# Kernel optimization log

Measured on AMD Instinct MI355X. Metric: run time of the kernel, lower is better.

## Reference

```python
import jax, jax.numpy as jnp
import numpy as np

T = 64        # n_estimators
DEPTH = 8
D = 2**DEPTH - 1   # internal nodes per tree (255)
K = 2**DEPTH       # leaves per tree (256)
M = 512       # n_features
C = 8         # class_num
B = 4096      # batch


def _build_path_masks():
    # Complete binary tree in heap order. For leaf l, walk from root;
    # going LEFT corresponds to b==+1 -> multiply (1 - x_node) -> Bpos,
    # going RIGHT corresponds to b==-1 -> multiply x_node -> Bneg.
    Bpos = np.zeros((K, D), dtype=np.float32)
    Bneg = np.zeros((K, D), dtype=np.float32)
    for l in range(K):
        node = 0
        for level in range(DEPTH):
            bit = (l >> (DEPTH - 1 - level)) & 1
            if bit == 0:
                Bpos[l, node] = 1.0
            else:
                Bneg[l, node] = 1.0
            node = 2 * node + 1 + bit
    return Bpos, Bneg


def setup_inputs() -> dict:
    rng = np.random.default_rng(0)
    key = jax.random.key(0)
    x = jax.random.normal(key, (B, M), dtype=jnp.float32)
    # fcn1: each internal node splits on one feature -> one-hot weight row,
    # bias = -threshold (change_parameters1).
    feat = rng.integers(0, M, size=(T, D))
    W1 = np.zeros((T, D, M), dtype=np.float32)
    W1[np.arange(T)[:, None], np.arange(D)[None, :], feat] = 1.0
    b1 = (-rng.standard_normal((T, D))).astype(np.float32)  # -threshold
    # Path masks shared across trees (complete trees), tiled per tree.
    Bpos1, Bneg1 = _build_path_masks()
    Bpos = np.broadcast_to(Bpos1, (T, K, D)).copy()
    Bneg = np.broadcast_to(Bneg1, (T, K, D)).copy()
    # fcn2 weight = c^T with zero bias (change_parameters2): leaf values [T, K, C]
    Cw = rng.random((T, K, C)).astype(np.float32)
    return {
        "input": x,
        "W1": jnp.asarray(W1),
        "b1": jnp.asarray(b1),
        "Bpos": jnp.asarray(Bpos),
        "Bneg": jnp.asarray(Bneg),
        "Cw": jnp.asarray(Cw),
    }


def reference(input, W1, b1, Bpos, Bneg, Cw):
    # z: [B, T, D] = 10 * (fcn1 per tree)
    z = 10.0 * (jnp.einsum("bm,tdm->btd", input, W1) + b1)
    # x = sigmoid(z); leaf-path product:
    #   x_c[b,t,k] = prod_d x^Bneg[t,k,d] * (1-x)^Bpos[t,k,d]
    # computed exactly in log-space (all factors in (0,1)):
    log_x = jax.nn.log_sigmoid(z)       # log sigmoid(z)
    log_1mx = jax.nn.log_sigmoid(-z)    # log (1 - sigmoid(z))
    log_xc = (jnp.einsum("btd,tkd->btk", log_x, Bneg)
              + jnp.einsum("btd,tkd->btk", log_1mx, Bpos))
    x_c = jnp.exp(log_xc)               # [B, T, K]
    # fcn2 (zero bias) then forest average over trees
    out = jnp.einsum("btk,tkc->bc", x_c, Cw) / T
    return out
```

## Files before the change

### kernel.cpp

```cpp
#include <hip/hip_runtime.h>
#include <hip/hip_bf16.h>

#define TT 64
#define DD 255
#define KK 256
#define MM 512
#define CC 8
#define BB 4096
#define NB 4
#define TPB 32
#define TG 4

typedef _Float16 h2 __attribute__((ext_vector_type(2)));

__device__ __forceinline__ float wave_sum(float v) {
    v += __shfl_down(v, 32, 64);
    v += __shfl_down(v, 16, 64);
    v += __shfl_down(v, 8, 64);
    v += __shfl_down(v, 4, 64);
    v += __shfl_down(v, 2, 64);
    v += __shfl_down(v, 1, 64);
    return v;
}

__global__ void feat_kernel(const float* __restrict__ W1, int* __restrict__ feat) {
    const int row = blockIdx.x * 4 + (threadIdx.x >> 6);
    const int lane = threadIdx.x & 63;
    const float4* r = reinterpret_cast<const float4*>(W1 + (size_t)row * MM);
    float4 a = r[lane];
    float4 b = r[lane + 64];
    float ba = (float)(4 * lane);
    float bb = (float)(4 * (lane + 64));
    float acc = 0.0f;
    acc = fmaf(a.x, ba,        acc);
    acc = fmaf(a.y, ba + 1.0f, acc);
    acc = fmaf(a.z, ba + 2.0f, acc);
    acc = fmaf(a.w, ba + 3.0f, acc);
    acc = fmaf(b.x, bb,        acc);
    acc = fmaf(b.y, bb + 1.0f, acc);
    acc = fmaf(b.z, bb + 2.0f, acc);
    acc = fmaf(b.w, bb + 3.0f, acc);
    acc = wave_sum(acc);
    if (lane == 0) feat[row] = (int)(acc + 0.5f);
}

__device__ __forceinline__ float sigm_from(float xv, float c1) {
    float earg = fmaf(-14.426950408889634f, xv, c1);
    float e = exp2f(earg);
    return __builtin_amdgcn_rcpf(1.0f + e);
}

__global__ __launch_bounds__(256, 2) void forest_kernel(
        const float* __restrict__ x, const float* __restrict__ b1,
        const float* __restrict__ Cw, const int* __restrict__ feat,
        float* __restrict__ out) {
    __shared__ float xsi[MM][NB];
    __shared__ h2 s8[NB * 2 * 256];
    __shared__ float red[4][NB][CC];

    const int tid = threadIdx.x;
    const int b0 = blockIdx.x * NB;
    const int t0 = blockIdx.y * TPB;

    for (int idx = tid; idx < MM * NB; idx += 256) {
        int m = idx & (MM - 1);
        int bl = idx >> 9;
        xsi[m][bl] = x[(size_t)(b0 + bl) * MM + m];
    }

    h2 acc[NB][4];
    #pragma unroll
    for (int bl = 0; bl < NB; ++bl)
        #pragma unroll
        for (int q = 0; q < 4; ++q)
            acc[bl][q] = (h2){(_Float16)0.0f, (_Float16)0.0f};

    const int i = tid & 127;
    const int sub = tid >> 7;
    const h2 one = {(_Float16)1.0f, (_Float16)1.0f};

    for (int g = 0; g < TPB / TG; ++g) {
        __syncthreads();
        if (tid < DD) {
            const int d = tid;
            int f[TG];
            float c1[TG];
            #pragma unroll
            for (int j = 0; j < TG; ++j) {
                int t = t0 + g * TG + j;
                f[j] = feat[t * DD + d];
                c1[j] = -14.426950408889634f * b1[t * DD + d];
            }
            float sv[NB][TG];
            #pragma unroll
            for (int j = 0; j < TG; ++j) {
                float4 xv = *reinterpret_cast<const float4*>(&xsi[f[j]][0]);
                sv[0][j] = sigm_from(xv.x, c1[j]);
                sv[1][j] = sigm_from(xv.y, c1[j]);
                sv[2][j] = sigm_from(xv.z, c1[j]);
                sv[3][j] = sigm_from(xv.w, c1[j]);
            }
            #pragma unroll
            for (int bl = 0; bl < NB; ++bl) {
                s8[(bl * 2 + 0) * 256 + d] =
                    (h2){(_Float16)sv[bl][0], (_Float16)sv[bl][1]};
                s8[(bl * 2 + 1) * 256 + d] =
                    (h2){(_Float16)sv[bl][2], (_Float16)sv[bl][3]};
            }
        }
        __syncthreads();

        h2 cwa[2][4], cwb[2][4];
        #pragma unroll
        for (int j = 0; j < 2; ++j) {
            int t = t0 + g * TG + sub * 2 + j;
            const float4* p = reinterpret_cast<const float4*>(
                Cw + ((size_t)t * KK + 2 * i) * CC);
            float4 a0 = p[0], a1 = p[1], bv0 = p[2], bv1 = p[3];
            cwa[j][0] = (h2){(_Float16)a0.x, (_Float16)a0.y};
            cwa[j][1] = (h2){(_Float16)a0.z, (_Float16)a0.w};
            cwa[j][2] = (h2){(_Float16)a1.x, (_Float16)a1.y};
            cwa[j][3] = (h2){(_Float16)a1.z, (_Float16)a1.w};
            cwb[j][0] = (h2){(_Float16)bv0.x, (_Float16)bv0.y};
            cwb[j][1] = (h2){(_Float16)bv0.z, (_Float16)bv0.w};
            cwb[j][2] = (h2){(_Float16)bv1.x, (_Float16)bv1.y};
            cwb[j][3] = (h2){(_Float16)bv1.z, (_Float16)bv1.w};
        }

        h2 pre[NB];
        #pragma unroll
        for (int bl = 0; bl < NB; ++bl) pre[bl] = one;

        #pragma unroll
        for (int lev = 0; lev < 7; ++lev) {
            int node = (1 << lev) - 1 + (i >> (7 - lev));
            int bit = (i >> (6 - lev)) & 1;
            _Float16 offs = (_Float16)(1 - bit);
            _Float16 sgs = (_Float16)(2 * bit - 1);
            h2 offv = {offs, offs};
            h2 sg = {sgs, sgs};
            #pragma unroll
            for (int bl = 0; bl < NB; ++bl) {
                h2 s = s8[(bl * 2 + sub) * 256 + node];
                pre[bl] *= (sg * s + offv);
            }
        }
        const int node7 = 127 + i;
        #pragma unroll
        for (int bl = 0; bl < NB; ++bl) {
            h2 s = s8[(bl * 2 + sub) * 256 + node7];
            h2 pe = pre[bl] * (one - s);
            h2 po = pre[bl] * s;
            #pragma unroll
            for (int q = 0; q < 4; ++q) {
                acc[bl][q] += (h2){pe.x, pe.x} * cwa[0][q];
                acc[bl][q] += (h2){po.x, po.x} * cwb[0][q];
                acc[bl][q] += (h2){pe.y, pe.y} * cwa[1][q];
                acc[bl][q] += (h2){po.y, po.y} * cwb[1][q];
            }
        }
    }

    const int lane = tid & 63;
    const int wv = tid >> 6;
    float af[NB][CC];
    #pragma unroll
    for (int bl = 0; bl < NB; ++bl) {
        #pragma unroll
        for (int q = 0; q < 4; ++q) {
            af[bl][2 * q]     = wave_sum((float)acc[bl][q].x);
            af[bl][2 * q + 1] = wave_sum((float)acc[bl][q].y);
        }
    }
    if (lane == 0) {
        #pragma unroll
        for (int bl = 0; bl < NB; ++bl)
            #pragma unroll
            for (int c = 0; c < CC; ++c)
                red[wv][bl][c] = af[bl][c];
    }
    __syncthreads();
    if (tid < NB * CC) {
        int bl = tid >> 3;
        int c = tid & 7;
        float s = red[0][bl][c] + red[1][bl][c] + red[2][bl][c] + red[3][bl][c];
        atomicAdd(&out[(size_t)(b0 + bl) * CC + c], s * (1.0f / 64.0f));
    }
}

extern "C" void kernel_launch(void* const* d_in, const int* in_sizes, int n_in,
                              void* d_out, int out_size, void* d_ws, size_t ws_size,
                              hipStream_t stream) {
    const float* x  = (const float*)d_in[0];
    const float* W1 = (const float*)d_in[1];
    const float* b1 = (const float*)d_in[2];
    const float* Cw = (const float*)d_in[5];
    float* out = (float*)d_out;
    int* feat = (int*)d_ws;

    hipMemsetAsync(out, 0, (size_t)BB * CC * sizeof(float), stream);
    feat_kernel<<<(TT * DD) / 4, 256, 0, stream>>>(W1, feat);
    forest_kernel<<<dim3(BB / NB, 2), 256, 0, stream>>>(x, b1, Cw, feat, out);
}
```

Baseline: 168.3 us.

## Compute leaf-weighted sums with MFMA, per-wave trees and 16-row batch tiles

The forest kernel is restructured so that each wave owns one tree at a time and processes 16 batch rows. Each lane expands a subtree of leaf probabilities in fp32 and packs them to fp16, then uses mfma_f32_16x16x32_f16 against fp16 leaf values staged in LDS. This replaces the packed-half FMA accumulation. Inputs are staged as fp16 and the grid becomes 256x4 blocks. The change aims to move the leaf-by-class contraction onto matrix cores and cut block-level syncs, at the cost of fp16 rounding of x and leaf values and of relying on intra-wave LDS ordering without barriers.

```diff
diff --git a/kernel.cpp b/kernel.cpp
--- a/kernel.cpp
+++ b/kernel.cpp
@@ -7,11 +7,16 @@
 #define MM 512
 #define CC 8
 #define BB 4096
-#define NB 4
-#define TPB 32
-#define TG 4
-
-typedef _Float16 h2 __attribute__((ext_vector_type(2)));
+#define RB 16
+#define TPB 16
+
+typedef _Float16 h8 __attribute__((ext_vector_type(8)));
+typedef _Float16 h2v __attribute__((ext_vector_type(2)));
+typedef float f4 __attribute__((ext_vector_type(4)));
+
+__device__ __forceinline__ h2v pkrtz(float a, float b) {
+    return __builtin_bit_cast(h2v, __builtin_amdgcn_cvt_pkrtz(a, b));
+}
 
 __device__ __forceinline__ float wave_sum(float v) {
     v += __shfl_down(v, 32, 64);
@@ -54,137 +59,162 @@
         const float* __restrict__ x, const float* __restrict__ b1,
         const float* __restrict__ Cw, const int* __restrict__ feat,
         float* __restrict__ out) {
-    __shared__ float xsi[MM][NB];
-    __shared__ h2 s8[NB * 2 * 256];
-    __shared__ float red[4][NB][CC];
+    __shared__ _Float16 xsi[MM * RB];
+    __shared__ _Float16 s8[4][256 * RB];
+    __shared__ _Float16 cwl[4][8 * 8 * 4 * 8];
+    __shared__ f4 red[4][64];
 
     const int tid = threadIdx.x;
-    const int b0 = blockIdx.x * NB;
+    const int w = tid >> 6;
+    const int lane = tid & 63;
+    const int b0 = blockIdx.x * RB;
     const int t0 = blockIdx.y * TPB;
-
-    for (int idx = tid; idx < MM * NB; idx += 256) {
-        int m = idx & (MM - 1);
-        int bl = idx >> 9;
-        xsi[m][bl] = x[(size_t)(b0 + bl) * MM + m];
-    }
-
-    h2 acc[NB][4];
-    #pragma unroll
-    for (int bl = 0; bl < NB; ++bl)
-        #pragma unroll
-        for (int q = 0; q < 4; ++q)
-            acc[bl][q] = (h2){(_Float16)0.0f, (_Float16)0.0f};
-
-    const int i = tid & 127;
-    const int sub = tid >> 7;
-    const h2 one = {(_Float16)1.0f, (_Float16)1.0f};
-
-    for (int g = 0; g < TPB / TG; ++g) {
-        __syncthreads();
-        if (tid < DD) {
-            const int d = tid;
-            int f[TG];
-            float c1[TG];
-            #pragma unroll
-            for (int j = 0; j < TG; ++j) {
-                int t = t0 + g * TG + j;
-                f[j] = feat[t * DD + d];
-                c1[j] = -14.426950408889634f * b1[t * DD + d];
-            }
-            float sv[NB][TG];
-            #pragma unroll
-            for (int j = 0; j < TG; ++j) {
-                float4 xv = *reinterpret_cast<const float4*>(&xsi[f[j]][0]);
-                sv[0][j] = sigm_from(xv.x, c1[j]);
-                sv[1][j] = sigm_from(xv.y, c1[j]);
-                sv[2][j] = sigm_from(xv.z, c1[j]);
-                sv[3][j] = sigm_from(xv.w, c1[j]);
-            }
-            #pragma unroll
-            for (int bl = 0; bl < NB; ++bl) {
-                s8[(bl * 2 + 0) * 256 + d] =
-                    (h2){(_Float16)sv[bl][0], (_Float16)sv[bl][1]};
-                s8[(bl * 2 + 1) * 256 + d] =
-                    (h2){(_Float16)sv[bl][2], (_Float16)sv[bl][3]};
-            }
-        }
-        __syncthreads();
-
-        h2 cwa[2][4], cwb[2][4];
-        #pragma unroll
-        for (int j = 0; j < 2; ++j) {
-            int t = t0 + g * TG + sub * 2 + j;
-            const float4* p = reinterpret_cast<const float4*>(
-                Cw + ((size_t)t * KK + 2 * i) * CC);
-            float4 a0 = p[0], a1 = p[1], bv0 = p[2], bv1 = p[3];
-            cwa[j][0] = (h2){(_Float16)a0.x, (_Float16)a0.y};
-            cwa[j][1] = (h2){(_Float16)a0.z, (_Float16)a0.w};
-            cwa[j][2] = (h2){(_Float16)a1.x, (_Float16)a1.y};
-            cwa[j][3] = (h2){(_Float16)a1.z, (_Float16)a1.w};
-            cwb[j][0] = (h2){(_Float16)bv0.x, (_Float16)bv0.y};
-            cwb[j][1] = (h2){(_Float16)bv0.z, (_Float16)bv0.w};
-            cwb[j][2] = (h2){(_Float16)bv1.x, (_Float16)bv1.y};
-            cwb[j][3] = (h2){(_Float16)bv1.z, (_Float16)bv1.w};
-        }
-
-        h2 pre[NB];
-        #pragma unroll
-        for (int bl = 0; bl < NB; ++bl) pre[bl] = one;
-
-        #pragma unroll
-        for (int lev = 0; lev < 7; ++lev) {
-            int node = (1 << lev) - 1 + (i >> (7 - lev));
-            int bit = (i >> (6 - lev)) & 1;
-            _Float16 offs = (_Float16)(1 - bit);
-            _Float16 sgs = (_Float16)(2 * bit - 1);
-            h2 offv = {offs, offs};
-            h2 sg = {sgs, sgs};
-            #pragma unroll
-            for (int bl = 0; bl < NB; ++bl) {
-                h2 s = s8[(bl * 2 + sub) * 256 + node];
-                pre[bl] *= (sg * s + offv);
-            }
-        }
-        const int node7 = 127 + i;
-        #pragma unroll
-        for (int bl = 0; bl < NB; ++bl) {
-            h2 s = s8[(bl * 2 + sub) * 256 + node7];
-            h2 pe = pre[bl] * (one - s);
-            h2 po = pre[bl] * s;
-            #pragma unroll
-            for (int q = 0; q < 4; ++q) {
-                acc[bl][q] += (h2){pe.x, pe.x} * cwa[0][q];
-                acc[bl][q] += (h2){po.x, po.x} * cwb[0][q];
-                acc[bl][q] += (h2){pe.y, pe.y} * cwa[1][q];
-                acc[bl][q] += (h2){po.y, po.y} * cwb[1][q];
-            }
-        }
-    }
-
-    const int lane = tid & 63;
-    const int wv = tid >> 6;
-    float af[NB][CC];
-    #pragma unroll
-    for (int bl = 0; bl < NB; ++bl) {
-        #pragma unroll
-        for (int q = 0; q < 4; ++q) {
-            af[bl][2 * q]     = wave_sum((float)acc[bl][q].x);
-            af[bl][2 * q + 1] = wave_sum((float)acc[bl][q].y);
-        }
-    }
-    if (lane == 0) {
-        #pragma unroll
-        for (int bl = 0; bl < NB; ++bl)
-            #pragma unroll
-            for (int c = 0; c < CC; ++c)
-                red[wv][bl][c] = af[bl][c];
+    const int m = lane & 15;
+    const int slot = lane >> 4;
+
+    for (int e = tid; e < RB * MM / 4; e += 256) {
+        int r = e >> 7;
+        int m4 = (e & 127) << 2;
+        float4 v = *reinterpret_cast<const float4*>(x + (size_t)(b0 + r) * MM + m4);
+        xsi[(m4 + 0) * RB + r] = (_Float16)v.x;
+        xsi[(m4 + 1) * RB + r] = (_Float16)v.y;
+        xsi[(m4 + 2) * RB + r] = (_Float16)v.z;
+        xsi[(m4 + 3) * RB + r] = (_Float16)v.w;
     }
     __syncthreads();
-    if (tid < NB * CC) {
-        int bl = tid >> 3;
-        int c = tid & 7;
-        float s = red[0][bl][c] + red[1][bl][c] + red[2][bl][c] + red[3][bl][c];
-        atomicAdd(&out[(size_t)(b0 + bl) * CC + c], s * (1.0f / 64.0f));
+
+    _Float16* s8w = s8[w];
+    _Float16* cww = cwl[w];
+
+    const int b3 = slot >> 1, b4 = slot & 1;
+    const float sg3 = (float)(2 * b3 - 1), off3 = (float)(1 - b3);
+    const float sg4 = (float)(2 * b4 - 1), off4 = (float)(1 - b4);
+
+    f4 acc = {0.f, 0.f, 0.f, 0.f};
+
+    for (int tt = 0; tt < 4; ++tt) {
+        const int t = t0 + w * 4 + tt;
+        asm volatile("" ::: "memory");
+
+        #pragma unroll
+        for (int kq = 0; kq < 4; ++kq) {
+            int d = kq * 64 + lane;
+            if (d < DD) {
+                int f = feat[t * DD + d];
+                float c1 = -14.426950408889634f * b1[t * DD + d];
+                const float4* xp = reinterpret_cast<const float4*>(xsi + f * RB);
+                float4 A = xp[0], Bv = xp[1];
+                float s[16];
+                h2v u;
+                u = __builtin_bit_cast(h2v, A.x);  s[0] = sigm_from((float)u.x, c1);  s[1] = sigm_from((float)u.y, c1);
+                u = __builtin_bit_cast(h2v, A.y);  s[2] = sigm_from((float)u.x, c1);  s[3] = sigm_from((float)u.y, c1);
+                u = __builtin_bit_cast(h2v, A.z);  s[4] = sigm_from((float)u.x, c1);  s[5] = sigm_from((float)u.y, c1);
+                u = __builtin_bit_cast(h2v, A.w);  s[6] = sigm_from((float)u.x, c1);  s[7] = sigm_from((float)u.y, c1);
+                u = __builtin_bit_cast(h2v, Bv.x); s[8] = sigm_from((float)u.x, c1);  s[9] = sigm_from((float)u.y, c1);
+                u = __builtin_bit_cast(h2v, Bv.y); s[10] = sigm_from((float)u.x, c1); s[11] = sigm_from((float)u.y, c1);
+                u = __builtin_bit_cast(h2v, Bv.z); s[12] = sigm_from((float)u.x, c1); s[13] = sigm_from((float)u.y, c1);
+                u = __builtin_bit_cast(h2v, Bv.w); s[14] = sigm_from((float)u.x, c1); s[15] = sigm_from((float)u.y, c1);
+                float4 W0, W1;
+                W0.x = __builtin_bit_cast(float, pkrtz(s[0], s[1]));
+                W0.y = __builtin_bit_cast(float, pkrtz(s[2], s[3]));
+                W0.z = __builtin_bit_cast(float, pkrtz(s[4], s[5]));
+                W0.w = __builtin_bit_cast(float, pkrtz(s[6], s[7]));
+                W1.x = __builtin_bit_cast(float, pkrtz(s[8], s[9]));
+                W1.y = __builtin_bit_cast(float, pkrtz(s[10], s[11]));
+                W1.z = __builtin_bit_cast(float, pkrtz(s[12], s[13]));
+                W1.w = __builtin_bit_cast(float, pkrtz(s[14], s[15]));
+                *reinterpret_cast<float4*>(s8w + d * RB) = W0;
+                *reinterpret_cast<float4*>(s8w + d * RB + 8) = W1;
+            }
+        }
+
+        #pragma unroll
+        for (int kq = 0; kq < 4; ++kq) {
+            int k = kq * 64 + lane;
+            const float4* cp = reinterpret_cast<const float4*>(Cw + ((size_t)t * KK + k) * CC);
+            float4 p0 = cp[0], p1 = cp[1];
+            int cc = k >> 5, sl = (k >> 3) & 3, j = k & 7;
+            _Float16* bp = cww + ((cc * 8) * 4 + sl) * 8 + j;
+            bp[0 * 32] = (_Float16)p0.x;
+            bp[1 * 32] = (_Float16)p0.y;
+            bp[2 * 32] = (_Float16)p0.z;
+            bp[3 * 32] = (_Float16)p0.w;
+            bp[4 * 32] = (_Float16)p1.x;
+            bp[5 * 32] = (_Float16)p1.y;
+            bp[6 * 32] = (_Float16)p1.z;
+            bp[7 * 32] = (_Float16)p1.w;
+        }
+        asm volatile("s_waitcnt lgkmcnt(0)" ::: "memory");
+
+        float s0 = (float)s8w[0 * RB + m];
+        float s1 = (float)s8w[1 * RB + m];
+        float s2 = (float)s8w[2 * RB + m];
+        float s3 = (float)s8w[3 * RB + m];
+        float s4 = (float)s8w[4 * RB + m];
+        float s5p = (float)s8w[5 * RB + m];
+        float s6 = (float)s8w[6 * RB + m];
+        float P10 = 1.0f - s0, P11 = s0;
+        float P200 = P10 * (1.0f - s1), P201 = P10 * s1;
+        float P210 = P11 * (1.0f - s2), P211 = P11 * s2;
+        float P3a[8];
+        P3a[0] = P200 * (1.0f - s3); P3a[1] = P200 * s3;
+        P3a[2] = P201 * (1.0f - s4); P3a[3] = P201 * s4;
+        P3a[4] = P210 * (1.0f - s5p); P3a[5] = P210 * s5p;
+        P3a[6] = P211 * (1.0f - s6); P3a[7] = P211 * s6;
+
+        #pragma unroll
+        for (int c = 0; c < 8; ++c) {
+            const int n3 = 7 + c;
+            float sc3 = (float)s8w[n3 * RB + m];
+            float f3 = fmaf(sg3, sc3, off3);
+            int n4 = 2 * n3 + 1 + b3;
+            float sc4 = (float)s8w[n4 * RB + m];
+            float f4v = fmaf(sg4, sc4, off4);
+            float P5 = P3a[c] * f3 * f4v;
+            int n5 = 2 * n4 + 1 + b4;
+            float s5 = (float)s8w[n5 * RB + m];
+            float v1 = P5 * s5, v0 = P5 - v1;
+            int q0 = 2 * n5 + 1;
+            float sq0 = (float)s8w[q0 * RB + m];
+            float sq1 = (float)s8w[(q0 + 1) * RB + m];
+            float w01 = v0 * sq0, w00 = v0 - w01;
+            float w11 = v1 * sq1, w10 = v1 - w11;
+            int r0 = 2 * q0 + 1;
+            float sr0 = (float)s8w[(r0 + 0) * RB + m];
+            float sr1 = (float)s8w[(r0 + 1) * RB + m];
+            float sr2 = (float)s8w[(r0 + 2) * RB + m];
+            float sr3 = (float)s8w[(r0 + 3) * RB + m];
+            float l1 = w00 * sr0, l0 = w00 - l1;
+            float l3 = w01 * sr1, l2 = w01 - l3;
+            float l5 = w10 * sr2, l4 = w10 - l5;
+            float l7 = w11 * sr3, l6 = w11 - l7;
+            union { h8 v; h2v p[4]; } U;
+            U.p[0] = pkrtz(l0, l1);
+            U.p[1] = pkrtz(l2, l3);
+            U.p[2] = pkrtz(l4, l5);
+            U.p[3] = pkrtz(l6, l7);
+            h8 bf = {};
+            if (m < CC)
+                bf = *reinterpret_cast<const h8*>(cww + ((c * 8 + m) * 4 + slot) * 8);
+            acc = __builtin_amdgcn_mfma_f32_16x16x32_f16(U.v, bf, acc, 0, 0, 0);
+        }
+    }
+
+    red[w][lane] = acc;
+    __syncthreads();
+    if (tid < 64) {
+        f4 sum = red[0][tid];
+        sum += red[1][tid];
+        sum += red[2][tid];
+        sum += red[3][tid];
+        int n = tid & 15, sl = tid >> 4;
+        if (n < CC) {
+            #pragma unroll
+            for (int reg = 0; reg < 4; ++reg) {
+                int row = sl * 4 + reg;
+                atomicAdd(&out[(size_t)(b0 + row) * CC + n], sum[reg] * (1.0f / 64.0f));
+            }
+        }
     }
 }
 
@@ -198,7 +228,7 @@
     float* out = (float*)d_out;
     int* feat = (int*)d_ws;
 
-    hipMemsetAsync(out, 0, (size_t)BB * CC * sizeof(float), stream);
+    (void)hipMemsetAsync(out, 0, (size_t)BB * CC * sizeof(float), stream);
     feat_kernel<<<(TT * DD) / 4, 256, 0, stream>>>(W1, feat);
-    forest_kernel<<<dim3(BB / NB, 2), 256, 0, stream>>>(x, b1, Cw, feat, out);
-}
+    forest_kernel<<<dim3(BB / RB, TT / TPB), 256, 0, stream>>>(x, b1, Cw, feat, out);
+}
```

Result: faster. 155.1 us (-7.8%).
